# Kernel tuning notes

Measured on AMD Instinct MI355X. Metric: run time of the kernel, lower is better.

## Reference

```python
import jax, jax.numpy as jnp
import numpy as np

DIM = 1024
KEY = 128
UV = 1024  # dim * mlp_ratio // 2
SCALE = 1.0 / np.sqrt(KEY).astype(np.float32)
NEG_INF = 1e12


def _sinusoidal(n, d):
    # RoPE tables: sin/cos of shape [n, d//2]
    pos = np.arange(n)[:, None].astype(np.float32)
    inv = (1.0 / 10000 ** (np.arange(0, d, 2).astype(np.float32) / d))[None, :]
    ang = pos * inv
    return jnp.asarray(np.sin(ang)), jnp.asarray(np.cos(ang))


def setup_inputs() -> dict:
    key = jax.random.key(0)
    ks = jax.random.split(key, 4)
    B, N = 4, 2048
    hidden_states = jax.random.normal(ks[0], (B, N, DIM), dtype=jnp.float32)
    attention_mask = jax.random.randint(ks[1], (B, N, N), 0, 2).astype(jnp.int32)
    sin, cos = _sinusoidal(N, KEY)
    Wi = jax.random.normal(ks[2], (DIM, UV * 2 + KEY), dtype=jnp.float32) * (DIM ** -0.5)
    bi = jnp.zeros((UV * 2 + KEY,), jnp.float32)
    Wo = jax.random.normal(ks[3], (UV, DIM), dtype=jnp.float32) * (UV ** -0.5)
    bo = jnp.zeros((DIM,), jnp.float32)
    return {
        "hidden_states": hidden_states, "attention_mask": attention_mask,
        "sin": sin, "cos": cos, "Wi": Wi, "bi": bi, "Wo": Wo, "bo": bo,
        "q_gamma": jnp.ones((KEY,), jnp.float32), "q_beta": jnp.zeros((KEY,), jnp.float32),
        "k_gamma": jnp.ones((KEY,), jnp.float32), "k_beta": jnp.zeros((KEY,), jnp.float32),
    }


def _rotary(x, sin, cos):
    # x: [b, n, d]; sin/cos: [n, d//2]; interleaved RoPE, concat layout
    x1, x2 = x[..., 0::2], x[..., 1::2]
    return jnp.concatenate([x1 * cos - x2 * sin, x1 * sin + x2 * cos], axis=-1)


def reference(hidden_states, attention_mask, sin, cos, Wi, bi, Wo, bo,
              q_gamma, q_beta, k_gamma, k_beta):
    x = jax.nn.silu(hidden_states @ Wi + bi)            # [b, n, 2176]
    u, v, qk = x[..., :UV], x[..., UV:2 * UV], x[..., 2 * UV:]
    q = _rotary(qk * q_gamma + q_beta, sin, cos)        # [b, n, 128]
    k = _rotary(qk * k_gamma + k_beta, sin, cos)
    a = jnp.einsum('bmd,bnd->bmn', q, k) * SCALE        # [b, m, n]
    mask = attention_mask != 0
    a = jnp.where(mask, a, -NEG_INF)
    ll = attention_mask.sum(-1, keepdims=True).astype(a.dtype)  # [b, m, 1]
    A = jnp.square(jax.nn.relu(a)) / ll                 # squared_relu normalize
    out = (u * jnp.einsum('bmn,bnd->bmd', A, v)) @ Wo + bo
    return out
```

## Files before the change

### kernel.cpp

```cpp
#include <hip/hip_runtime.h>
#include <hip/hip_bf16.h>
#include <cstdint>

#define DIM   1024
#define KEY   128
#define UV    1024
#define NCOL  (UV*2 + KEY)
#define SEQ   2048
#define BATCH 4
#define MTOT  (BATCH*SEQ)
#define SCALE 0.08838834764831845f

typedef __attribute__((ext_vector_type(8))) short short8;
typedef __attribute__((ext_vector_type(4))) float f32x4;

__device__ inline unsigned short f2b(float x) {
  unsigned int u = __float_as_uint(x);
  unsigned int r = (u + 0x7fffu + ((u >> 16) & 1u)) >> 16;
  return (unsigned short)r;
}
__device__ inline float b2f(unsigned short x) {
  return __uint_as_float(((unsigned int)x) << 16);
}

__device__ inline void gload_lds16(const void* g, void* l) {
  __builtin_amdgcn_global_load_lds(
      (const __attribute__((address_space(1))) unsigned int*)g,
      (__attribute__((address_space(3))) unsigned int*)l, 16, 0, 0);
}

__device__ __forceinline__ void gemm128(
    const unsigned short* __restrict__ A, int lda,
    const unsigned short* __restrict__ Bt, int ldb,
    int K, f32x4 acc[4][4], unsigned short* lds) {
  const int tid  = threadIdx.x;
  const int lane = tid & 63;
  const int wid  = tid >> 6;
  const int wr   = wid >> 1, wc = wid & 1;
  const int fr   = lane & 15;
  const int fq   = lane >> 4;

#pragma unroll
  for (int i = 0; i < 4; ++i)
#pragma unroll
    for (int j = 0; j < 4; ++j) acc[i][j] = (f32x4){0.f, 0.f, 0.f, 0.f};

  auto stage = [&](int k, int d) {
    unsigned short* la = lds + d * 8192;
    unsigned short* lb = la + 4096;
#pragma unroll
    for (int p = 0; p < 2; ++p) {
      int c = p * 256 + tid;
      int r = c >> 2, q = c & 3;
      int qs = q ^ ((r >> 1) & 3);
      gload_lds16(A + (size_t)r * lda + k * 32 + qs * 8,
                  la + (size_t)(p * 256 + wid * 64) * 8);
    }
#pragma unroll
    for (int p = 0; p < 2; ++p) {
      int c = p * 256 + tid;
      int r = c >> 2, q = c & 3;
      int qs = q ^ ((r >> 1) & 3);
      gload_lds16(Bt + (size_t)r * ldb + k * 32 + qs * 8,
                  lb + (size_t)(p * 256 + wid * 64) * 8);
    }
  };

  const int slot = (fq ^ ((fr >> 1) & 3)) * 8;
  const int rA   = (wr * 64 + fr) * 32 + slot;
  const int rB   = (wc * 64 + fr) * 32 + slot;

  const int NK = K >> 5;
  stage(0, 0);
  for (int k = 0; k < NK; ++k) {
    const int d = k & 1;
    if (k + 1 < NK) {
      stage(k + 1, d ^ 1);
      asm volatile("s_waitcnt vmcnt(4)" ::: "memory");
    } else {
      asm volatile("s_waitcnt vmcnt(0)" ::: "memory");
    }
    __builtin_amdgcn_s_barrier();
    asm volatile("" ::: "memory");
    const unsigned short* la = lds + d * 8192;
    const unsigned short* lb = la + 4096;
    short8 af[4], bf[4];
#pragma unroll
    for (int s = 0; s < 4; ++s) {
      af[s] = *(const short8*)&la[rA + s * 512];
      bf[s] = *(const short8*)&lb[rB + s * 512];
    }
#pragma unroll
    for (int i = 0; i < 4; ++i)
#pragma unroll
      for (int j = 0; j < 4; ++j)
        acc[i][j] = __builtin_amdgcn_mfma_f32_16x16x32_bf16(af[i], bf[j], acc[i][j], 0, 0, 0);
    asm volatile("" ::: "memory");
    __builtin_amdgcn_s_barrier();
    asm volatile("" ::: "memory");
  }
}

#define EPILOGUE_COORDS()                      \
  const int lane = threadIdx.x & 63;           \
  const int wid  = threadIdx.x >> 6;           \
  const int wr   = wid >> 1, wc = wid & 1;     \
  const int fr   = lane & 15;                  \
  const int fq   = lane >> 4;

__device__ __forceinline__ void xcd_swz(int& tx, int& ty) {
  const int gx = gridDim.x, gy = gridDim.y;
  const int n = gx * gy;
  const int D = blockIdx.y * gx + blockIdx.x;
  const int c = (D & 7) * (n >> 3) + (D >> 3);
  tx = c / gy;
  ty = c - tx * gy;
}

__global__ __launch_bounds__(256) void k_cvt(const float* __restrict__ in,
                                             unsigned short* __restrict__ out) {
  int id = blockIdx.x * 256 + threadIdx.x;
  float4 f = ((const float4*)in)[id];
  ushort4 o;
  o.x = f2b(f.x); o.y = f2b(f.y); o.z = f2b(f.z); o.w = f2b(f.w);
  ((ushort4*)out)[id] = o;
}

__global__ void k_tcvt(const float* __restrict__ in, unsigned short* __restrict__ out,
                       int R, int C) {
  __shared__ float t[32][33];
  int c0 = blockIdx.x * 32, r0 = blockIdx.y * 32;
  int tx = threadIdx.x, ty = threadIdx.y;
#pragma unroll
  for (int i = 0; i < 4; ++i)
    t[ty + i * 8][tx] = in[(size_t)(r0 + ty + i * 8) * C + c0 + tx];
  __syncthreads();
#pragma unroll
  for (int i = 0; i < 4; ++i)
    out[(size_t)(c0 + ty + i * 8) * R + r0 + tx] = f2b(t[tx][ty + i * 8]);
}

__global__ __launch_bounds__(256) void k_maskprep(const int* __restrict__ mask,
                                                  float* __restrict__ ll,
                                                  unsigned int* __restrict__ mb) {
  int wid = threadIdx.x >> 6, lane = threadIdx.x & 63;
  int row = blockIdx.x * 4 + wid;
  const int4* p = (const int4*)(mask + (size_t)row * SEQ);
  int s = 0;
#pragma unroll
  for (int i = 0; i < 8; ++i) {
    int4 v = p[i * 64 + lane];
    unsigned nib = (v.x != 0 ? 1u : 0u) | (v.y != 0 ? 2u : 0u) |
                   (v.z != 0 ? 4u : 0u) | (v.w != 0 ? 8u : 0u);
    unsigned w = 0;
#pragma unroll
    for (int k2 = 0; k2 < 8; ++k2)
      w |= __shfl(nib, (lane & ~7) + k2, 64) << (4 * k2);
    if ((lane & 7) == 0) mb[(size_t)row * 64 + i * 8 + (lane >> 3)] = w;
    s += v.x + v.y + v.z + v.w;
  }
  for (int off = 32; off; off >>= 1) s += __shfl_down(s, off);
  if (lane == 0) ll[row] = (float)s;
}

__global__ __launch_bounds__(256) void k_rope(const float* __restrict__ qk,
                                              const float* __restrict__ sn,
                                              const float* __restrict__ cs,
                                              const float* __restrict__ qg,
                                              const float* __restrict__ qb,
                                              const float* __restrict__ kg,
                                              const float* __restrict__ kb,
                                              unsigned short* __restrict__ q,
                                              unsigned short* __restrict__ k) {
  int id = blockIdx.x * 256 + threadIdx.x;
  int m = id >> 6, t = id & 63;
  int n = m & (SEQ - 1);
  float x1 = qk[m * KEY + 2 * t], x2 = qk[m * KEY + 2 * t + 1];
  float s_ = sn[n * 64 + t], c_ = cs[n * 64 + t];
  float a1 = x1 * qg[2 * t] + qb[2 * t];
  float a2 = x2 * qg[2 * t + 1] + qb[2 * t + 1];
  q[m * KEY + t]      = f2b(a1 * c_ - a2 * s_);
  q[m * KEY + 64 + t] = f2b(a1 * s_ + a2 * c_);
  float b1 = x1 * kg[2 * t] + kb[2 * t];
  float b2 = x2 * kg[2 * t + 1] + kb[2 * t + 1];
  k[m * KEY + t]      = f2b(b1 * c_ - b2 * s_);
  k[m * KEY + 64 + t] = f2b(b1 * s_ + b2 * c_);
}

__global__ __launch_bounds__(256) void k_vT(const unsigned short* __restrict__ v,
                                            unsigned short* __restrict__ vT) {
  __shared__ unsigned short t[64][65];
  int b = blockIdx.z;
  int n0 = blockIdx.x * 64;
  int d0 = blockIdx.y * 64;
  int tid = threadIdx.x;
  int r = tid >> 4;
  int c4 = (tid & 15) * 4;
#pragma unroll
  for (int i = 0; i < 4; ++i) {
    int n = n0 + r + i * 16;
    ushort4 val = *(const ushort4*)&v[((size_t)b * SEQ + n) * UV + d0 + c4];
    t[c4 + 0][r + i * 16] = val.x;
    t[c4 + 1][r + i * 16] = val.y;
    t[c4 + 2][r + i * 16] = val.z;
    t[c4 + 3][r + i * 16] = val.w;
  }
  __syncthreads();
#pragma unroll
  for (int i = 0; i < 4; ++i) {
    int d = d0 + r + i * 16;
    ushort4 o;
    o.x = t[r + i * 16][c4 + 0];
    o.y = t[r + i * 16][c4 + 1];
    o.z = t[r + i * 16][c4 + 2];
    o.w = t[r + i * 16][c4 + 3];
    *(ushort4*)&vT[((size_t)b * UV + d) * SEQ + n0 + c4] = o;
  }
}

__global__ __launch_bounds__(256, 4) void k_gemm1(const unsigned short* __restrict__ hbf,
                                                  const unsigned short* __restrict__ WiT,
                                                  const float* __restrict__ bi,
                                                  unsigned short* __restrict__ u,
                                                  unsigned short* __restrict__ v,
                                                  float* __restrict__ qk) {
  __shared__ unsigned short lds[16384];
  int tx, ty; xcd_swz(tx, ty);
  int m0 = tx * 128, n0 = ty * 128;
  f32x4 acc[4][4];
  gemm128(hbf + (size_t)m0 * DIM, DIM, WiT + (size_t)n0 * DIM, DIM, DIM, acc, lds);
  EPILOGUE_COORDS();
#pragma unroll
  for (int i = 0; i < 4; ++i)
#pragma unroll
    for (int j = 0; j < 4; ++j)
#pragma unroll
      for (int r = 0; r < 4; ++r) {
        int row = m0 + wr * 64 + i * 16 + fq * 4 + r;
        int col = n0 + wc * 64 + j * 16 + fr;
        float x = acc[i][j][r] + bi[col];
        float s = x / (1.f + __expf(-x));
        if (n0 < UV)            u[(size_t)row * UV + col] = f2b(s);
        else if (n0 < 2 * UV)   v[(size_t)row * UV + col - UV] = f2b(s);
        else                    qk[(size_t)row * KEY + col - 2 * UV] = s;
      }
}

__global__ __launch_bounds__(256, 4) void k_qk(const unsigned short* __restrict__ q,
                                               const unsigned short* __restrict__ k,
                                               const unsigned int* __restrict__ mb,
                                               const float* __restrict__ ll,
                                               unsigned short* __restrict__ Abuf) {
  __shared__ unsigned short lds[16384];
  int b = blockIdx.z;
  int tx, ty; xcd_swz(tx, ty);
  int m0 = tx * 128, n0 = ty * 128;
  f32x4 acc[4][4];
  gemm128(q + ((size_t)b * SEQ + m0) * KEY, KEY,
          k + ((size_t)b * SEQ + n0) * KEY, KEY, KEY, acc, lds);
  EPILOGUE_COORDS();
#pragma unroll
  for (int i = 0; i < 4; ++i)
#pragma unroll
    for (int r = 0; r < 4; ++r) {
      int row = m0 + wr * 64 + i * 16 + fq * 4 + r;
      size_t rb = (size_t)b * SEQ + row;
      unsigned long long mw =
          *(const unsigned long long*)&mb[rb * 64 + (n0 >> 5) + wc * 2];
      float rll = 1.0f / ll[rb];
#pragma unroll
      for (int j = 0; j < 4; ++j) {
        int col = n0 + wc * 64 + j * 16 + fr;
        float a = acc[i][j][r] * SCALE;
        bool on = (mw >> (j * 16 + fr)) & 1ull;
        float rel = (on && a > 0.f) ? a : 0.f;
        Abuf[rb * SEQ + col] = f2b(rel * rel * rll);
      }
    }
}

__global__ __launch_bounds__(256, 4) void k_av(const unsigned short* __restrict__ Abuf,
                                               const unsigned short* __restrict__ vT,
                                               const unsigned short* __restrict__ u,
                                               unsigned short* __restrict__ g) {
  __shared__ unsigned short lds[16384];
  int b = blockIdx.z;
  int tx, ty; xcd_swz(tx, ty);
  int m0 = tx * 128, n0 = ty * 128;
  f32x4 acc[4][4];
  gemm128(Abuf + ((size_t)b * SEQ + m0) * SEQ, SEQ,
          vT + ((size_t)b * UV + n0) * SEQ, SEQ, SEQ, acc, lds);
  EPILOGUE_COORDS();
#pragma unroll
  for (int i = 0; i < 4; ++i)
#pragma unroll
    for (int j = 0; j < 4; ++j)
#pragma unroll
      for (int r = 0; r < 4; ++r) {
        int row = m0 + wr * 64 + i * 16 + fq * 4 + r;
        int col = n0 + wc * 64 + j * 16 + fr;
        size_t gi = ((size_t)b * SEQ + row) * UV + col;
        g[gi] = f2b(acc[i][j][r] * b2f(u[gi]));
      }
}

__global__ __launch_bounds__(256, 4) void k_out(const unsigned short* __restrict__ g,
                                                const unsigned short* __restrict__ WoT,
                                                const float* __restrict__ bo,
                                                float* __restrict__ out) {
  __shared__ unsigned short lds[16384];
  int tx, ty; xcd_swz(tx, ty);
  int m0 = tx * 128, n0 = ty * 128;
  f32x4 acc[4][4];
  gemm128(g + (size_t)m0 * UV, UV, WoT + (size_t)n0 * UV, UV, UV, acc, lds);
  EPILOGUE_COORDS();
#pragma unroll
  for (int i = 0; i < 4; ++i)
#pragma unroll
    for (int j = 0; j < 4; ++j)
#pragma unroll
      for (int r = 0; r < 4; ++r) {
        int row = m0 + wr * 64 + i * 16 + fq * 4 + r;
        int col = n0 + wc * 64 + j * 16 + fr;
        out[(size_t)row * DIM + col] = acc[i][j][r] + bo[col];
      }
}

extern "C" void kernel_launch(void* const* d_in, const int* in_sizes, int n_in,
                              void* d_out, int out_size, void* d_ws, size_t ws_size,
                              hipStream_t stream) {
  const float* h    = (const float*)d_in[0];
  const int*   mask = (const int*)d_in[1];
  const float* sn   = (const float*)d_in[2];
  const float* cs   = (const float*)d_in[3];
  const float* Wi   = (const float*)d_in[4];
  const float* bi   = (const float*)d_in[5];
  const float* Wo   = (const float*)d_in[6];
  const float* bo   = (const float*)d_in[7];
  const float* qg   = (const float*)d_in[8];
  const float* qb   = (const float*)d_in[9];
  const float* kg   = (const float*)d_in[10];
  const float* kb   = (const float*)d_in[11];
  float* out = (float*)d_out;

  char* ws = (char*)d_ws;
  size_t off = 0;
  auto alloc = [&](size_t bytes) { void* p = ws + off; off += (bytes + 255) & ~(size_t)255; return p; };
  unsigned short* hbf  = (unsigned short*)alloc((size_t)MTOT * DIM * 2);
  unsigned short* WiT  = (unsigned short*)alloc((size_t)NCOL * DIM * 2);
  unsigned short* WoT  = (unsigned short*)alloc((size_t)DIM * UV * 2);
  unsigned short* u    = (unsigned short*)alloc((size_t)MTOT * UV * 2);
  unsigned short* v    = (unsigned short*)alloc((size_t)MTOT * UV * 2);
  unsigned short* vT   = (unsigned short*)alloc((size_t)MTOT * UV * 2);
  float*          qkb  = (float*)alloc((size_t)MTOT * KEY * 4);
  unsigned short* qbuf = (unsigned short*)alloc((size_t)MTOT * KEY * 2);
  unsigned short* kbuf = (unsigned short*)alloc((size_t)MTOT * KEY * 2);
  float*          ll   = (float*)alloc((size_t)MTOT * 4);
  unsigned int*   mbits= (unsigned int*)alloc((size_t)MTOT * 64 * 4);
  unsigned short* Abuf = (unsigned short*)alloc((size_t)BATCH * SEQ * SEQ * 2);
  unsigned short* g    = (unsigned short*)alloc((size_t)MTOT * UV * 2);

  k_cvt<<<(MTOT * DIM / 4) / 256, 256, 0, stream>>>(h, hbf);
  k_tcvt<<<dim3(NCOL / 32, DIM / 32), dim3(32, 8), 0, stream>>>(Wi, WiT, DIM, NCOL);
  k_tcvt<<<dim3(UV / 32, DIM / 32), dim3(32, 8), 0, stream>>>(Wo, WoT, DIM, UV);
  k_maskprep<<<MTOT / 4, 256, 0, stream>>>(mask, ll, mbits);

  k_gemm1<<<dim3(MTOT / 128, NCOL / 128), 256, 0, stream>>>(hbf, WiT, bi, u, v, qkb);
  k_rope<<<(MTOT * 64) / 256, 256, 0, stream>>>(qkb, sn, cs, qg, qb, kg, kb, qbuf, kbuf);
  k_vT<<<dim3(SEQ / 64, UV / 64, BATCH), 256, 0, stream>>>(v, vT);
  k_qk<<<dim3(SEQ / 128, SEQ / 128, BATCH), 256, 0, stream>>>(qbuf, kbuf, mbits, ll, Abuf);
  k_av<<<dim3(SEQ / 128, UV / 128, BATCH), 256, 0, stream>>>(Abuf, vT, u, g);
  k_out<<<dim3(MTOT / 128, DIM / 128), 256, 0, stream>>>(g, WoT, bo, out);
}
```

Measured before the change: 190.2 us.

## Use 256x128 GEMM tiles with triple-buffered LDS pipeline

Replaces the shared 128x128 GEMM core with a 256x128 tile in which each of the four waves computes a 128x64 sub-tile (8x4 MFMA fragments). It adds three-stage LDS buffering, issuing loads two k-steps ahead with a single barrier per iteration, and raises wave priority around the MFMA block. All four GEMM kernels use this core, with dynamic LDS of 72KB and launch bounds lowered to 2 blocks per CU. The aim is more operand reuse per LDS load and better hiding of global load latency. The cost is higher register pressure, fewer resident blocks and half as many workgroups per grid.

```diff
diff --git a/kernel.cpp b/kernel.cpp
--- a/kernel.cpp
+++ b/kernel.cpp
@@ -29,27 +29,32 @@
       (__attribute__((address_space(3))) unsigned int*)l, 16, 0, 0);
 }
 
-__device__ __forceinline__ void gemm128(
+#define BARX() do { asm volatile("" ::: "memory"); __builtin_amdgcn_s_barrier(); asm volatile("" ::: "memory"); } while (0)
+
+__device__ __forceinline__ void gemm4w(
     const unsigned short* __restrict__ A, int lda,
     const unsigned short* __restrict__ Bt, int ldb,
-    int K, f32x4 acc[4][4], unsigned short* lds) {
+    int K, f32x4 acc[8][4], unsigned short* lds) {
   const int tid  = threadIdx.x;
   const int lane = tid & 63;
   const int wid  = tid >> 6;
-  const int wr   = wid >> 1, wc = wid & 1;
+  const int wm   = wid >> 1, wn = wid & 1;
   const int fr   = lane & 15;
   const int fq   = lane >> 4;
 
-#pragma unroll
-  for (int i = 0; i < 4; ++i)
+  unsigned short* ldsA = lds;
+  unsigned short* ldsB = lds + 3 * 8192;
+
+#pragma unroll
+  for (int i = 0; i < 8; ++i)
 #pragma unroll
     for (int j = 0; j < 4; ++j) acc[i][j] = (f32x4){0.f, 0.f, 0.f, 0.f};
 
   auto stage = [&](int k, int d) {
-    unsigned short* la = lds + d * 8192;
-    unsigned short* lb = la + 4096;
-#pragma unroll
-    for (int p = 0; p < 2; ++p) {
+    unsigned short* la = ldsA + d * 8192;
+    unsigned short* lb = ldsB + d * 4096;
+#pragma unroll
+    for (int p = 0; p < 4; ++p) {
       int c = p * 256 + tid;
       int r = c >> 2, q = c & 3;
       int qs = q ^ ((r >> 1) & 3);
@@ -67,44 +72,44 @@
   };
 
   const int slot = (fq ^ ((fr >> 1) & 3)) * 8;
-  const int rA   = (wr * 64 + fr) * 32 + slot;
-  const int rB   = (wc * 64 + fr) * 32 + slot;
+  const int aoff = (wm * 128 + fr) * 32 + slot;
+  const int boff = (wn * 64 + fr) * 32 + slot;
 
   const int NK = K >> 5;
   stage(0, 0);
+  stage(1, 1);
+  asm volatile("s_waitcnt vmcnt(6)" ::: "memory");
+
+  int dcur = 0, d2 = 2;
   for (int k = 0; k < NK; ++k) {
-    const int d = k & 1;
-    if (k + 1 < NK) {
-      stage(k + 1, d ^ 1);
-      asm volatile("s_waitcnt vmcnt(4)" ::: "memory");
-    } else {
-      asm volatile("s_waitcnt vmcnt(0)" ::: "memory");
-    }
-    __builtin_amdgcn_s_barrier();
-    asm volatile("" ::: "memory");
-    const unsigned short* la = lds + d * 8192;
-    const unsigned short* lb = la + 4096;
-    short8 af[4], bf[4];
-#pragma unroll
-    for (int s = 0; s < 4; ++s) {
-      af[s] = *(const short8*)&la[rA + s * 512];
-      bf[s] = *(const short8*)&lb[rB + s * 512];
-    }
-#pragma unroll
-    for (int i = 0; i < 4; ++i)
+    BARX();
+    if (k + 2 < NK) stage(k + 2, d2);
+    const unsigned short* la = ldsA + dcur * 8192;
+    const unsigned short* lb = ldsB + dcur * 4096;
+    short8 af[8], bf[4];
+#pragma unroll
+    for (int i = 0; i < 8; ++i) af[i] = *(const short8*)&la[aoff + i * 512];
+#pragma unroll
+    for (int j = 0; j < 4; ++j) bf[j] = *(const short8*)&lb[boff + j * 512];
+    __builtin_amdgcn_s_setprio(1);
+#pragma unroll
+    for (int i = 0; i < 8; ++i)
 #pragma unroll
       for (int j = 0; j < 4; ++j)
         acc[i][j] = __builtin_amdgcn_mfma_f32_16x16x32_bf16(af[i], bf[j], acc[i][j], 0, 0, 0);
+    __builtin_amdgcn_s_setprio(0);
     asm volatile("" ::: "memory");
-    __builtin_amdgcn_s_barrier();
-    asm volatile("" ::: "memory");
+    if (k + 2 < NK)      asm volatile("s_waitcnt vmcnt(6)" ::: "memory");
+    else if (k + 1 < NK) asm volatile("s_waitcnt vmcnt(0)" ::: "memory");
+    dcur = (dcur == 2) ? 0 : dcur + 1;
+    d2   = (d2 == 2)   ? 0 : d2 + 1;
   }
 }
 
 #define EPILOGUE_COORDS()                      \
   const int lane = threadIdx.x & 63;           \
   const int wid  = threadIdx.x >> 6;           \
-  const int wr   = wid >> 1, wc = wid & 1;     \
+  const int wm   = wid >> 1, wn = wid & 1;     \
   const int fr   = lane & 15;                  \
   const int fq   = lane >> 4;
 
@@ -218,59 +223,61 @@
   }
 }
 
-__global__ __launch_bounds__(256, 4) void k_gemm1(const unsigned short* __restrict__ hbf,
+#define LDS_BYTES 73728
+
+__global__ __launch_bounds__(256, 2) void k_gemm1(const unsigned short* __restrict__ hbf,
                                                   const unsigned short* __restrict__ WiT,
                                                   const float* __restrict__ bi,
                                                   unsigned short* __restrict__ u,
                                                   unsigned short* __restrict__ v,
                                                   float* __restrict__ qk) {
-  __shared__ unsigned short lds[16384];
+  extern __shared__ unsigned short lds[];
   int tx, ty; xcd_swz(tx, ty);
-  int m0 = tx * 128, n0 = ty * 128;
-  f32x4 acc[4][4];
-  gemm128(hbf + (size_t)m0 * DIM, DIM, WiT + (size_t)n0 * DIM, DIM, DIM, acc, lds);
+  int m0 = tx * 256, n0 = ty * 128;
+  f32x4 acc[8][4];
+  gemm4w(hbf + (size_t)m0 * DIM, DIM, WiT + (size_t)n0 * DIM, DIM, DIM, acc, lds);
   EPILOGUE_COORDS();
 #pragma unroll
-  for (int i = 0; i < 4; ++i)
+  for (int i = 0; i < 8; ++i)
 #pragma unroll
     for (int j = 0; j < 4; ++j)
 #pragma unroll
       for (int r = 0; r < 4; ++r) {
-        int row = m0 + wr * 64 + i * 16 + fq * 4 + r;
-        int col = n0 + wc * 64 + j * 16 + fr;
+        int row = m0 + wm * 128 + i * 16 + fq * 4 + r;
+        int col = n0 + wn * 64 + j * 16 + fr;
         float x = acc[i][j][r] + bi[col];
         float s = x / (1.f + __expf(-x));
-        if (n0 < UV)            u[(size_t)row * UV + col] = f2b(s);
-        else if (n0 < 2 * UV)   v[(size_t)row * UV + col - UV] = f2b(s);
-        else                    qk[(size_t)row * KEY + col - 2 * UV] = s;
+        if (col < UV)            u[(size_t)row * UV + col] = f2b(s);
+        else if (col < 2 * UV)   v[(size_t)row * UV + col - UV] = f2b(s);
+        else                     qk[(size_t)row * KEY + col - 2 * UV] = s;
       }
 }
 
-__global__ __launch_bounds__(256, 4) void k_qk(const unsigned short* __restrict__ q,
+__global__ __launch_bounds__(256, 2) void k_qk(const unsigned short* __restrict__ q,
                                                const unsigned short* __restrict__ k,
                                                const unsigned int* __restrict__ mb,
                                                const float* __restrict__ ll,
                                                unsigned short* __restrict__ Abuf) {
-  __shared__ unsigned short lds[16384];
+  extern __shared__ unsigned short lds[];
   int b = blockIdx.z;
   int tx, ty; xcd_swz(tx, ty);
-  int m0 = tx * 128, n0 = ty * 128;
-  f32x4 acc[4][4];
-  gemm128(q + ((size_t)b * SEQ + m0) * KEY, KEY,
-          k + ((size_t)b * SEQ + n0) * KEY, KEY, KEY, acc, lds);
+  int m0 = tx * 256, n0 = ty * 128;
+  f32x4 acc[8][4];
+  gemm4w(q + ((size_t)b * SEQ + m0) * KEY, KEY,
+         k + ((size_t)b * SEQ + n0) * KEY, KEY, KEY, acc, lds);
   EPILOGUE_COORDS();
 #pragma unroll
-  for (int i = 0; i < 4; ++i)
+  for (int i = 0; i < 8; ++i)
 #pragma unroll
     for (int r = 0; r < 4; ++r) {
-      int row = m0 + wr * 64 + i * 16 + fq * 4 + r;
+      int row = m0 + wm * 128 + i * 16 + fq * 4 + r;
       size_t rb = (size_t)b * SEQ + row;
       unsigned long long mw =
-          *(const unsigned long long*)&mb[rb * 64 + (n0 >> 5) + wc * 2];
+          *(const unsigned long long*)&mb[rb * 64 + (n0 >> 5) + wn * 2];
       float rll = 1.0f / ll[rb];
 #pragma unroll
       for (int j = 0; j < 4; ++j) {
-        int col = n0 + wc * 64 + j * 16 + fr;
+        int col = n0 + wn * 64 + j * 16 + fr;
         float a = acc[i][j][r] * SCALE;
         bool on = (mw >> (j * 16 + fr)) & 1ull;
         float rel = (on && a > 0.f) ? a : 0.f;
@@ -279,49 +286,49 @@
     }
 }
 
-__global__ __launch_bounds__(256, 4) void k_av(const unsigned short* __restrict__ Abuf,
+__global__ __launch_bounds__(256, 2) void k_av(const unsigned short* __restrict__ Abuf,
                                                const unsigned short* __restrict__ vT,
                                                const unsigned short* __restrict__ u,
                                                unsigned short* __restrict__ g) {
-  __shared__ unsigned short lds[16384];
+  extern __shared__ unsigned short lds[];
   int b = blockIdx.z;
   int tx, ty; xcd_swz(tx, ty);
-  int m0 = tx * 128, n0 = ty * 128;
-  f32x4 acc[4][4];
-  gemm128(Abuf + ((size_t)b * SEQ + m0) * SEQ, SEQ,
-          vT + ((size_t)b * UV + n0) * SEQ, SEQ, SEQ, acc, lds);
+  int m0 = tx * 256, n0 = ty * 128;
+  f32x4 acc[8][4];
+  gemm4w(Abuf + ((size_t)b * SEQ + m0) * SEQ, SEQ,
+         vT + ((size_t)b * UV + n0) * SEQ, SEQ, SEQ, acc, lds);
   EPILOGUE_COORDS();
 #pragma unroll
-  for (int i = 0; i < 4; ++i)
+  for (int i = 0; i < 8; ++i)
 #pragma unroll
     for (int j = 0; j < 4; ++j)
 #pragma unroll
       for (int r = 0; r < 4; ++r) {
-        int row = m0 + wr * 64 + i * 16 + fq * 4 + r;
-        int col = n0 + wc * 64 + j * 16 + fr;
+        int row = m0 + wm * 128 + i * 16 + fq * 4 + r;
+        int col = n0 + wn * 64 + j * 16 + fr;
         size_t gi = ((size_t)b * SEQ + row) * UV + col;
         g[gi] = f2b(acc[i][j][r] * b2f(u[gi]));
       }
 }
 
-__global__ __launch_bounds__(256, 4) void k_out(const unsigned short* __restrict__ g,
+__global__ __launch_bounds__(256, 2) void k_out(const unsigned short* __restrict__ g,
                                                 const unsigned short* __restrict__ WoT,
                                                 const float* __restrict__ bo,
                                                 float* __restrict__ out) {
-  __shared__ unsigned short lds[16384];
+  extern __shared__ unsigned short lds[];
   int tx, ty; xcd_swz(tx, ty);
-  int m0 = tx * 128, n0 = ty * 128;
-  f32x4 acc[4][4];
-  gemm128(g + (size_t)m0 * UV, UV, WoT + (size_t)n0 * UV, UV, UV, acc, lds);
+  int m0 = tx * 256, n0 = ty * 128;
+  f32x4 acc[8][4];
+  gemm4w(g + (size_t)m0 * UV, UV, WoT + (size_t)n0 * UV, UV, UV, acc, lds);
   EPILOGUE_COORDS();
 #pragma unroll
-  for (int i = 0; i < 4; ++i)
+  for (int i = 0; i < 8; ++i)
 #pragma unroll
     for (int j = 0; j < 4; ++j)
 #pragma unroll
       for (int r = 0; r < 4; ++r) {
-        int row = m0 + wr * 64 + i * 16 + fq * 4 + r;
-        int col = n0 + wc * 64 + j * 16 + fr;
+        int row = m0 + wm * 128 + i * 16 + fq * 4 + r;
+        int col = n0 + wn * 64 + j * 16 + fr;
         out[(size_t)row * DIM + col] = acc[i][j][r] + bo[col];
       }
 }
@@ -343,6 +350,11 @@
   const float* kb   = (const float*)d_in[11];
   float* out = (float*)d_out;
 
+  hipFuncSetAttribute((const void*)k_gemm1, hipFuncAttributeMaxDynamicSharedMemorySize, LDS_BYTES);
+  hipFuncSetAttribute((const void*)k_qk,    hipFuncAttributeMaxDynamicSharedMemorySize, LDS_BYTES);
+  hipFuncSetAttribute((const void*)k_av,    hipFuncAttributeMaxDynamicSharedMemorySize, LDS_BYTES);
+  hipFuncSetAttribute((const void*)k_out,   hipFuncAttributeMaxDynamicSharedMemorySize, LDS_BYTES);
+
   char* ws = (char*)d_ws;
   size_t off = 0;
   auto alloc = [&](size_t bytes) { void* p = ws + off; off += (bytes + 255) & ~(size_t)255; return p; };
@@ -365,10 +377,10 @@
   k_tcvt<<<dim3(UV / 32, DIM / 32), dim3(32, 8), 0, stream>>>(Wo, WoT, DIM, UV);
   k_maskprep<<<MTOT / 4, 256, 0, stream>>>(mask, ll, mbits);
 
-  k_gemm1<<<dim3(MTOT / 128, NCOL / 128), 256, 0, stream>>>(hbf, WiT, bi, u, v, qkb);
+  k_gemm1<<<dim3(MTOT / 256, NCOL / 128), 256, LDS_BYTES, stream>>>(hbf, WiT, bi, u, v, qkb);
   k_rope<<<(MTOT * 64) / 256, 256, 0, stream>>>(qkb, sn, cs, qg, qb, kg, kb, qbuf, kbuf);
   k_vT<<<dim3(SEQ / 64, UV / 64, BATCH), 256, 0, stream>>>(v, vT);
-  k_qk<<<dim3(SEQ / 128, SEQ / 128, BATCH), 256, 0, stream>>>(qbuf, kbuf, mbits, ll, Abuf);
-  k_av<<<dim3(SEQ / 128, UV / 128, BATCH), 256, 0, stream>>>(Abuf, vT, u, g);
-  k_out<<<dim3(MTOT / 128, DIM / 128), 256, 0, stream>>>(g, WoT, bo, out);
-}
+  k_qk<<<dim3(SEQ / 256, SEQ / 128, BATCH), 256, LDS_BYTES, stream>>>(qbuf, kbuf, mbits, ll, Abuf);
+  k_av<<<dim3(SEQ / 256, UV / 128, BATCH), 256, LDS_BYTES, stream>>>(Abuf, vT, u, g);
+  k_out<<<dim3(MTOT / 256, DIM / 128), 256, LDS_BYTES, stream>>>(g, WoT, bo, out);
+}
```

New measurement: 258.5 us. 35.9% more time.
